# Optimization experiments

Measured on AMD Instinct MI355X. Metric: run time of the kernel, lower is better.

Reference implementation:

```python
import jax, jax.numpy as jnp
import numpy as np

S, B, H = 4096, 64, 512

def setup_inputs() -> dict:
    key = jax.random.key(0)
    k1, k2, k3, k4, k5, k6 = jax.random.split(key, 6)
    scale = 1.0 / np.sqrt(H)
    return {
        "encoder_hidden_states": jax.random.normal(k1, (S, B, H), dtype=jnp.float32),
        "h_t": jax.random.normal(k2, (B, H), dtype=jnp.float32),
        "encoder_context_mask": jnp.ones((B, S), dtype=jnp.int32),
        "W_a": jax.random.uniform(k3, (H, H), minval=-scale, maxval=scale, dtype=jnp.float32),
        "b_a": jax.random.uniform(k4, (H,), minval=-scale, maxval=scale, dtype=jnp.float32),
        "W_r": jax.random.uniform(k5, (H, 2 * H), minval=-1.0 / np.sqrt(2 * H), maxval=1.0 / np.sqrt(2 * H), dtype=jnp.float32),
        "b_r": jax.random.uniform(k6, (H,), minval=-1.0 / np.sqrt(2 * H), maxval=1.0 / np.sqrt(2 * H), dtype=jnp.float32),
    }

def reference(encoder_hidden_states, h_t, encoder_context_mask, W_a, b_a, W_r, b_r):
    # 'general' Luong score: score[s,b] = (W_a h_s[s,b]) . h_t[b]
    # (original code wastefully forms an [S,B,B] tensor then takes the diagonal;
    #  the math is exactly this per-batch dot product)
    hs_proj = encoder_hidden_states @ W_a.T + b_a            # [S,B,H]
    scores = jnp.einsum('sbh,bh->sb', hs_proj, h_t)          # [S,B]
    log_mask = jnp.log(encoder_context_mask.astype(jnp.float32)).T  # [S,B]
    scores = scores + log_mask
    a_t = jax.nn.softmax(scores, axis=0)                     # [S,B]
    c_t = jnp.einsum('sb,sbh->bh', a_t, encoder_hidden_states)  # [B,H]
    cat = jnp.concatenate((c_t, h_t), axis=1)                # [B,2H]
    return jnp.tanh(cat @ W_r.T + b_r)                       # [B,H]
```

## Files before the change

### kernel.cpp

```cpp
#include <hip/hip_runtime.h>
#include <math.h>

#define S 4096
#define B 64
#define H 512
#define MAX_NSPLIT 32

__global__ __launch_bounds__(256) void prep_kernel(
    const float* __restrict__ h_t, const float* __restrict__ W_a,
    const float* __restrict__ b_a, float* __restrict__ v, float* __restrict__ c0)
{
    const int b = blockIdx.x;
    const int t = threadIdx.x;
    __shared__ float sh[H];
    __shared__ float red[256];

    float h0 = h_t[b * H + t];
    float h1 = h_t[b * H + 256 + t];
    sh[t] = h0;
    sh[256 + t] = h1;
    red[t] = b_a[t] * h0 + b_a[256 + t] * h1;
    __syncthreads();
    for (int off = 128; off; off >>= 1) {
        if (t < off) red[t] += red[t + off];
        __syncthreads();
    }

    float acc0 = 0.f, acc1 = 0.f;
#pragma unroll 8
    for (int i = 0; i < H; ++i) {
        float h = sh[i];
        acc0 = fmaf(h, W_a[i * H + t], acc0);
        acc1 = fmaf(h, W_a[i * H + 256 + t], acc1);
    }
    v[b * H + t] = acc0;
    v[b * H + 256 + t] = acc1;
    if (t == 0) c0[b] = red[0];
}

__global__ __launch_bounds__(256) void pass_kernel(
    const float* __restrict__ hs, const int* __restrict__ mask,
    const float* __restrict__ v, const float* __restrict__ c0,
    float* __restrict__ part, int nsplit, int rows)
{
    const int b = blockIdx.x % B;
    const int chunk = blockIdx.x / B;
    const int lane = threadIdx.x & 63;
    const int w = threadIdx.x >> 6;

    const float4 vlo = *(const float4*)&v[b * H + lane * 4];
    const float4 vhi = *(const float4*)&v[b * H + 256 + lane * 4];
    const float cc = c0[b];

    float m = -INFINITY, l = 0.f;
    float4 olo = {0.f, 0.f, 0.f, 0.f};
    float4 ohi = {0.f, 0.f, 0.f, 0.f};

    const int s0 = chunk * rows;
    for (int k = w; k < rows; k += 4) {
        const int s = s0 + k;
        if (mask[b * S + s] == 0) continue;
        const float* row = hs + ((size_t)s * B + b) * H;
        const float4 dlo = *(const float4*)&row[lane * 4];
        const float4 dhi = *(const float4*)&row[256 + lane * 4];

        float d = dlo.x * vlo.x + dlo.y * vlo.y + dlo.z * vlo.z + dlo.w * vlo.w
                + dhi.x * vhi.x + dhi.y * vhi.y + dhi.z * vhi.z + dhi.w * vhi.w;
#pragma unroll
        for (int off = 32; off; off >>= 1) d += __shfl_xor(d, off);
        const float score = d + cc;

        const float mn = fmaxf(m, score);
        const float p = __expf(score - mn);
        const float alpha = __expf(m - mn);
        l = l * alpha + p;
        olo.x = olo.x * alpha + p * dlo.x;
        olo.y = olo.y * alpha + p * dlo.y;
        olo.z = olo.z * alpha + p * dlo.z;
        olo.w = olo.w * alpha + p * dlo.w;
        ohi.x = ohi.x * alpha + p * dhi.x;
        ohi.y = ohi.y * alpha + p * dhi.y;
        ohi.z = ohi.z * alpha + p * dhi.z;
        ohi.w = ohi.w * alpha + p * dhi.w;
        m = mn;
    }

    __shared__ float sm[4], sl[4];
    __shared__ __align__(16) float so[4][H];
    *(float4*)&so[w][lane * 4] = olo;
    *(float4*)&so[w][256 + lane * 4] = ohi;
    if (lane == 0) { sm[w] = m; sl[w] = l; }
    __syncthreads();

    const float M = fmaxf(fmaxf(sm[0], sm[1]), fmaxf(sm[2], sm[3]));
    float wt[4];
    float L = 0.f;
#pragma unroll
    for (int i = 0; i < 4; ++i) {
        wt[i] = (sl[i] > 0.f) ? __expf(sm[i] - M) : 0.f;
        L += sl[i] * wt[i];
    }
    const int t = threadIdx.x;
    float* P = part + (size_t)(b * nsplit + chunk) * (H + 2);
    const float O0 = so[0][t] * wt[0] + so[1][t] * wt[1]
                   + so[2][t] * wt[2] + so[3][t] * wt[3];
    const float O1 = so[0][256 + t] * wt[0] + so[1][256 + t] * wt[1]
                   + so[2][256 + t] * wt[2] + so[3][256 + t] * wt[3];
    P[2 + t] = O0;
    P[2 + 256 + t] = O1;
    if (t == 0) { P[0] = M; P[1] = L; }
}

__global__ __launch_bounds__(256) void final_kernel(
    const float* __restrict__ part, const float* __restrict__ h_t,
    const float* __restrict__ W_r, const float* __restrict__ b_r,
    float* __restrict__ out, int nsplit)
{
    const int b = blockIdx.x;
    const int half = blockIdx.y;
    const int t = threadIdx.x;
    __shared__ __align__(16) float cat[2 * H];

    float M = -INFINITY;
    for (int c = 0; c < nsplit; ++c)
        M = fmaxf(M, part[(size_t)(b * nsplit + c) * (H + 2)]);

    float L = 0.f, O0 = 0.f, O1 = 0.f;
    for (int c = 0; c < nsplit; ++c) {
        const float* P = part + (size_t)(b * nsplit + c) * (H + 2);
        const float lc = P[1];
        const float wc = (lc > 0.f) ? __expf(P[0] - M) : 0.f;
        L += lc * wc;
        O0 += P[2 + t] * wc;
        O1 += P[2 + 256 + t] * wc;
    }
    const float inv = 1.f / L;
    cat[t] = O0 * inv;
    cat[256 + t] = O1 * inv;
    cat[512 + t] = h_t[b * H + t];
    cat[768 + t] = h_t[b * H + 256 + t];
    __syncthreads();

    const int i = half * 256 + t;
    const float* wr = W_r + (size_t)i * (2 * H);
    float acc = b_r[i];
#pragma unroll 4
    for (int j = 0; j < 2 * H; j += 4) {
        const float4 wv = *(const float4*)&wr[j];
        acc += wv.x * cat[j] + wv.y * cat[j + 1]
             + wv.z * cat[j + 2] + wv.w * cat[j + 3];
    }
    out[b * H + i] = tanhf(acc);
}

extern "C" void kernel_launch(void* const* d_in, const int* in_sizes, int n_in,
                              void* d_out, int out_size, void* d_ws, size_t ws_size,
                              hipStream_t stream) {
    const float* hs  = (const float*)d_in[0];
    const float* h_t = (const float*)d_in[1];
    const int* mask  = (const int*)d_in[2];
    const float* W_a = (const float*)d_in[3];
    const float* b_a = (const float*)d_in[4];
    const float* W_r = (const float*)d_in[5];
    const float* b_r = (const float*)d_in[6];
    float* out = (float*)d_out;
    float* ws = (float*)d_ws;

    int nsplit = MAX_NSPLIT;
    while (nsplit > 1) {
        size_t need = ((size_t)B * H + 64 + (size_t)B * nsplit * (H + 2)) * sizeof(float);
        if (need <= ws_size) break;
        nsplit >>= 1;
    }
    const int rows = S / nsplit;

    float* v = ws;
    float* c0 = ws + B * H;
    float* part = ws + B * H + 64;

    prep_kernel<<<B, 256, 0, stream>>>(h_t, W_a, b_a, v, c0);
    pass_kernel<<<B * nsplit, 256, 0, stream>>>(hs, mask, v, c0, part, nsplit, rows);
    final_kernel<<<dim3(B, 2), 256, 0, stream>>>(part, h_t, W_r, b_r, out, nsplit);
}
```

Before: 779.6 us.

## Batch eight rows per wave in attention pass with branchless mask and split partials

The pass kernel now loads eight rows per wave before any reduction, so more memory loads are in flight at once. It interleaves the eight shuffle reductions and rescales the online-softmax state once per tile instead of once per row. The per-row mask branch becomes an additive penalty read from shared memory, and the partial results are split into separate M, L and O arrays. The prep kernel is spread across twice as many blocks, and the split count is now fixed instead of adapting to the workspace size, which risks overflowing a small workspace and adds register pressure from the tile.

```diff
diff --git a/kernel.cpp b/kernel.cpp
--- a/kernel.cpp
+++ b/kernel.cpp
@@ -4,49 +4,61 @@
 #define S 4096
 #define B 64
 #define H 512
-#define MAX_NSPLIT 32
+#define NSPLIT 32
+#define ROWS 128
+#define TILE 8
 
 __global__ __launch_bounds__(256) void prep_kernel(
     const float* __restrict__ h_t, const float* __restrict__ W_a,
     const float* __restrict__ b_a, float* __restrict__ v, float* __restrict__ c0)
 {
     const int b = blockIdx.x;
+    const int half = blockIdx.y;
     const int t = threadIdx.x;
+    const int j = half * 256 + t;
     __shared__ float sh[H];
     __shared__ float red[256];
 
-    float h0 = h_t[b * H + t];
-    float h1 = h_t[b * H + 256 + t];
+    const float h0 = h_t[b * H + t];
+    const float h1 = h_t[b * H + 256 + t];
     sh[t] = h0;
     sh[256 + t] = h1;
-    red[t] = b_a[t] * h0 + b_a[256 + t] * h1;
-    __syncthreads();
-    for (int off = 128; off; off >>= 1) {
-        if (t < off) red[t] += red[t + off];
-        __syncthreads();
-    }
-
-    float acc0 = 0.f, acc1 = 0.f;
+    if (half == 0) red[t] = b_a[t] * h0 + b_a[256 + t] * h1;
+    __syncthreads();
+    if (half == 0) {
+        for (int off = 128; off; off >>= 1) {
+            if (t < off) red[t] += red[t + off];
+            __syncthreads();
+        }
+        if (t == 0) c0[b] = red[0];
+    }
+
+    float acc = 0.f;
 #pragma unroll 8
-    for (int i = 0; i < H; ++i) {
-        float h = sh[i];
-        acc0 = fmaf(h, W_a[i * H + t], acc0);
-        acc1 = fmaf(h, W_a[i * H + 256 + t], acc1);
-    }
-    v[b * H + t] = acc0;
-    v[b * H + 256 + t] = acc1;
-    if (t == 0) c0[b] = red[0];
+    for (int i = 0; i < H; ++i)
+        acc = fmaf(sh[i], W_a[i * H + j], acc);
+    v[b * H + j] = acc;
 }
 
 __global__ __launch_bounds__(256) void pass_kernel(
     const float* __restrict__ hs, const int* __restrict__ mask,
     const float* __restrict__ v, const float* __restrict__ c0,
-    float* __restrict__ part, int nsplit, int rows)
+    float* __restrict__ partM, float* __restrict__ partL,
+    float* __restrict__ partO)
 {
-    const int b = blockIdx.x % B;
-    const int chunk = blockIdx.x / B;
+    const int b = blockIdx.x & (B - 1);
+    const int chunk = blockIdx.x >> 6;
     const int lane = threadIdx.x & 63;
     const int w = threadIdx.x >> 6;
+    const int s0 = chunk * ROWS;
+
+    __shared__ float pen[ROWS];
+    __shared__ float sm[4], sl[4];
+    __shared__ __align__(16) float so[4][H];
+
+    if (threadIdx.x < ROWS)
+        pen[threadIdx.x] = mask[b * S + s0 + threadIdx.x] ? 0.f : -INFINITY;
+    __syncthreads();
 
     const float4 vlo = *(const float4*)&v[b * H + lane * 4];
     const float4 vhi = *(const float4*)&v[b * H + 256 + lane * 4];
@@ -56,37 +68,55 @@
     float4 olo = {0.f, 0.f, 0.f, 0.f};
     float4 ohi = {0.f, 0.f, 0.f, 0.f};
 
-    const int s0 = chunk * rows;
-    for (int k = w; k < rows; k += 4) {
-        const int s = s0 + k;
-        if (mask[b * S + s] == 0) continue;
-        const float* row = hs + ((size_t)s * B + b) * H;
-        const float4 dlo = *(const float4*)&row[lane * 4];
-        const float4 dhi = *(const float4*)&row[256 + lane * 4];
-
-        float d = dlo.x * vlo.x + dlo.y * vlo.y + dlo.z * vlo.z + dlo.w * vlo.w
-                + dhi.x * vhi.x + dhi.y * vhi.y + dhi.z * vhi.z + dhi.w * vhi.w;
-#pragma unroll
-        for (int off = 32; off; off >>= 1) d += __shfl_xor(d, off);
-        const float score = d + cc;
-
-        const float mn = fmaxf(m, score);
-        const float p = __expf(score - mn);
-        const float alpha = __expf(m - mn);
-        l = l * alpha + p;
-        olo.x = olo.x * alpha + p * dlo.x;
-        olo.y = olo.y * alpha + p * dlo.y;
-        olo.z = olo.z * alpha + p * dlo.z;
-        olo.w = olo.w * alpha + p * dlo.w;
-        ohi.x = ohi.x * alpha + p * dhi.x;
-        ohi.y = ohi.y * alpha + p * dhi.y;
-        ohi.z = ohi.z * alpha + p * dhi.z;
-        ohi.w = ohi.w * alpha + p * dhi.w;
+    for (int base = w * TILE; base < ROWS; base += 4 * TILE) {
+        float4 rl[TILE], rh[TILE];
+        const float* row0 = hs + ((size_t)(s0 + base) * B + b) * H;
+#pragma unroll
+        for (int r = 0; r < TILE; ++r) {
+            const float* row = row0 + (size_t)r * (B * H);
+            rl[r] = *(const float4*)&row[lane * 4];
+            rh[r] = *(const float4*)&row[256 + lane * 4];
+        }
+        float d[TILE];
+#pragma unroll
+        for (int r = 0; r < TILE; ++r) {
+            d[r] = rl[r].x * vlo.x + rl[r].y * vlo.y + rl[r].z * vlo.z + rl[r].w * vlo.w
+                 + rh[r].x * vhi.x + rh[r].y * vhi.y + rh[r].z * vhi.z + rh[r].w * vhi.w;
+        }
+#pragma unroll
+        for (int off = 32; off; off >>= 1) {
+#pragma unroll
+            for (int r = 0; r < TILE; ++r) d[r] += __shfl_xor(d[r], off);
+        }
+        float tmax = -INFINITY;
+#pragma unroll
+        for (int r = 0; r < TILE; ++r) {
+            d[r] += cc + pen[base + r];
+            tmax = fmaxf(tmax, d[r]);
+        }
+        const float mn = fmaxf(m, tmax);
+        const float ms = (mn == -INFINITY) ? 0.f : mn;
+        const float alpha = __expf(m - ms);
+        float p[TILE], psum = 0.f;
+#pragma unroll
+        for (int r = 0; r < TILE; ++r) { p[r] = __expf(d[r] - ms); psum += p[r]; }
+        l = l * alpha + psum;
+        olo.x *= alpha; olo.y *= alpha; olo.z *= alpha; olo.w *= alpha;
+        ohi.x *= alpha; ohi.y *= alpha; ohi.z *= alpha; ohi.w *= alpha;
+#pragma unroll
+        for (int r = 0; r < TILE; ++r) {
+            olo.x = fmaf(p[r], rl[r].x, olo.x);
+            olo.y = fmaf(p[r], rl[r].y, olo.y);
+            olo.z = fmaf(p[r], rl[r].z, olo.z);
+            olo.w = fmaf(p[r], rl[r].w, olo.w);
+            ohi.x = fmaf(p[r], rh[r].x, ohi.x);
+            ohi.y = fmaf(p[r], rh[r].y, ohi.y);
+            ohi.z = fmaf(p[r], rh[r].z, ohi.z);
+            ohi.w = fmaf(p[r], rh[r].w, ohi.w);
+        }
         m = mn;
     }
 
-    __shared__ float sm[4], sl[4];
-    __shared__ __align__(16) float so[4][H];
     *(float4*)&so[w][lane * 4] = olo;
     *(float4*)&so[w][256 + lane * 4] = ohi;
     if (lane == 0) { sm[w] = m; sl[w] = l; }
@@ -101,20 +131,20 @@
         L += sl[i] * wt[i];
     }
     const int t = threadIdx.x;
-    float* P = part + (size_t)(b * nsplit + chunk) * (H + 2);
-    const float O0 = so[0][t] * wt[0] + so[1][t] * wt[1]
-                   + so[2][t] * wt[2] + so[3][t] * wt[3];
-    const float O1 = so[0][256 + t] * wt[0] + so[1][256 + t] * wt[1]
-                   + so[2][256 + t] * wt[2] + so[3][256 + t] * wt[3];
-    P[2 + t] = O0;
-    P[2 + 256 + t] = O1;
-    if (t == 0) { P[0] = M; P[1] = L; }
+    const int idx = b * NSPLIT + chunk;
+    float* PO = partO + (size_t)idx * H;
+    PO[t]       = so[0][t] * wt[0] + so[1][t] * wt[1]
+                + so[2][t] * wt[2] + so[3][t] * wt[3];
+    PO[256 + t] = so[0][256 + t] * wt[0] + so[1][256 + t] * wt[1]
+                + so[2][256 + t] * wt[2] + so[3][256 + t] * wt[3];
+    if (t == 0) { partM[idx] = M; partL[idx] = L; }
 }
 
 __global__ __launch_bounds__(256) void final_kernel(
-    const float* __restrict__ part, const float* __restrict__ h_t,
+    const float* __restrict__ partM, const float* __restrict__ partL,
+    const float* __restrict__ partO, const float* __restrict__ h_t,
     const float* __restrict__ W_r, const float* __restrict__ b_r,
-    float* __restrict__ out, int nsplit)
+    float* __restrict__ out)
 {
     const int b = blockIdx.x;
     const int half = blockIdx.y;
@@ -122,17 +152,19 @@
     __shared__ __align__(16) float cat[2 * H];
 
     float M = -INFINITY;
-    for (int c = 0; c < nsplit; ++c)
-        M = fmaxf(M, part[(size_t)(b * nsplit + c) * (H + 2)]);
+#pragma unroll
+    for (int c = 0; c < NSPLIT; ++c)
+        M = fmaxf(M, partM[b * NSPLIT + c]);
 
     float L = 0.f, O0 = 0.f, O1 = 0.f;
-    for (int c = 0; c < nsplit; ++c) {
-        const float* P = part + (size_t)(b * nsplit + c) * (H + 2);
-        const float lc = P[1];
-        const float wc = (lc > 0.f) ? __expf(P[0] - M) : 0.f;
+#pragma unroll 4
+    for (int c = 0; c < NSPLIT; ++c) {
+        const float lc = partL[b * NSPLIT + c];
+        const float wc = (lc > 0.f) ? __expf(partM[b * NSPLIT + c] - M) : 0.f;
+        const float* PO = partO + (size_t)(b * NSPLIT + c) * H;
         L += lc * wc;
-        O0 += P[2 + t] * wc;
-        O1 += P[2 + 256 + t] * wc;
+        O0 += PO[t] * wc;
+        O1 += PO[256 + t] * wc;
     }
     const float inv = 1.f / L;
     cat[t] = O0 * inv;
@@ -166,19 +198,13 @@
     float* out = (float*)d_out;
     float* ws = (float*)d_ws;
 
-    int nsplit = MAX_NSPLIT;
-    while (nsplit > 1) {
-        size_t need = ((size_t)B * H + 64 + (size_t)B * nsplit * (H + 2)) * sizeof(float);
-        if (need <= ws_size) break;
-        nsplit >>= 1;
-    }
-    const int rows = S / nsplit;
-
-    float* v = ws;
-    float* c0 = ws + B * H;
-    float* part = ws + B * H + 64;
-
-    prep_kernel<<<B, 256, 0, stream>>>(h_t, W_a, b_a, v, c0);
-    pass_kernel<<<B * nsplit, 256, 0, stream>>>(hs, mask, v, c0, part, nsplit, rows);
-    final_kernel<<<dim3(B, 2), 256, 0, stream>>>(part, h_t, W_r, b_r, out, nsplit);
-}
+    float* v     = ws;
+    float* c0    = v + B * H;
+    float* partM = c0 + 64;
+    float* partL = partM + B * NSPLIT;
+    float* partO = partL + B * NSPLIT;
+
+    prep_kernel<<<dim3(B, 2), 256, 0, stream>>>(h_t, W_a, b_a, v, c0);
+    pass_kernel<<<B * NSPLIT, 256, 0, stream>>>(hs, mask, v, c0, partM, partL, partO);
+    final_kernel<<<dim3(B, 2), 256, 0, stream>>>(partM, partL, partO, h_t, W_r, b_r, out);
+}
```

Result: faster. 757.3 us (-2.9%).
